# Kernel tuning notes

Hardware: AMD Instinct MI355X
Metric: run time of the kernel (lower is better)

Reference implementation:

```python
import jax, jax.numpy as jnp
import numpy as np

N = 50000
D = 128
E = 600000
R = 8


def setup_inputs() -> dict:
    key = jax.random.key(0)
    ks = jax.random.split(key, 8)
    x = jax.random.normal(ks[0], (N, D), dtype=jnp.float32)
    edge_index = jax.random.randint(ks[1], (2, E), 0, N, dtype=jnp.int64)
    edge_type = jax.random.randint(ks[2], (E,), 0, R, dtype=jnp.int64)
    scale = 1.0 / np.sqrt(D)
    w1 = jax.random.normal(ks[3], (R, D, D), dtype=jnp.float32) * scale
    root1 = jax.random.normal(ks[4], (D, D), dtype=jnp.float32) * scale
    b1 = jnp.zeros((D,), dtype=jnp.float32)
    w2 = jax.random.normal(ks[5], (R, D, D), dtype=jnp.float32) * scale
    root2 = jax.random.normal(ks[6], (D, D), dtype=jnp.float32) * scale
    b2 = jnp.zeros((D,), dtype=jnp.float32)
    return {"x": x, "edge_index": edge_index, "edge_type": edge_type,
            "w1": w1, "root1": root1, "b1": b1,
            "w2": w2, "root2": root2, "b2": b2}


def _rgcn_conv(x, edge_index, edge_type, w, root, b):
    # PyG RGCNConv: per-relation MEAN aggregation of source features over
    # incoming edges, then relation-specific linear, summed over relations,
    # plus root transform and bias.
    src, dst = edge_index[0], edge_index[1]
    # combined segment id: (dst_node, relation) -> one segment_sum pass
    seg = dst * R + edge_type  # [E]
    msgs = x[src]              # [E, D] gather
    sums = jax.ops.segment_sum(msgs, seg, num_segments=N * R).reshape(N, R, D)
    cnts = jax.ops.segment_sum(jnp.ones((msgs.shape[0],), dtype=x.dtype), seg,
                               num_segments=N * R).reshape(N, R, 1)
    mean = sums / jnp.maximum(cnts, 1.0)  # [N, R, D]; empty -> 0
    out = jnp.einsum('nrd,rde->ne', mean, w) + x @ root + b
    return out


def reference(x, edge_index, edge_type, w1, root1, b1, w2, root2, b2):
    # dropout is identity in eval mode
    h = jax.nn.relu(_rgcn_conv(x, edge_index, edge_type, w1, root1, b1))
    out = jax.nn.relu(_rgcn_conv(h, edge_index, edge_type, w2, root2, b2))
    return out
```

## Files before the change

kernel.cpp:

```cpp
#include <hip/hip_runtime.h>

#define NN 50000
#define D 128
#define EE 600000
#define R 8
#define NR (NN * R)
#define SCAN_CHUNK 1024
#define NSB ((NR + SCAN_CHUNK - 1) / SCAN_CHUNK)
#define KT 36

typedef unsigned short u16;
typedef unsigned int u32;
typedef __attribute__((ext_vector_type(8))) short bf16x8;
typedef __attribute__((ext_vector_type(4))) float f32x4;

#define RDL(v_, i_) __builtin_amdgcn_readlane((int)(v_), (i_))

__device__ inline u16 f2bf(float f) {
    union { float f; u32 u; } v; v.f = f;
    return (u16)((v.u + 0x7FFFu + ((v.u >> 16) & 1u)) >> 16);
}
__device__ inline float bf2f(u16 h) {
    union { u32 u; float f; } v; v.u = ((u32)h) << 16;
    return v.f;
}

__global__ __launch_bounds__(256) void prep2_kernel(const float4* __restrict__ x,
                                                    u32* __restrict__ xb,
                                                    const int* __restrict__ dst,
                                                    const int* __restrict__ et,
                                                    int* __restrict__ cnt,
                                                    int* __restrict__ rk) {
    const int i = blockIdx.x * 256 + threadIdx.x;
    const float4 v = x[i];
    if (i < EE) rk[i] = atomicAdd(&cnt[dst[i] * R + et[i]], 1);
    xb[i * 2] = (u32)f2bf(v.x) | ((u32)f2bf(v.y) << 16);
    xb[i * 2 + 1] = (u32)f2bf(v.z) | ((u32)f2bf(v.w) << 16);
}

__global__ __launch_bounds__(256) void scanA(const int* __restrict__ cnt,
                                             int* __restrict__ off,
                                             int* __restrict__ bsum) {
    __shared__ int ts[256];
    const int b = blockIdx.x, t = threadIdx.x;
    const int base = b * SCAN_CHUNK + t * 4;
    int v0 = 0, v1 = 0, v2 = 0, v3 = 0;
    if (base + 3 < NR) {
        int4 q = *(const int4*)(cnt + base);
        v0 = q.x; v1 = q.y; v2 = q.z; v3 = q.w;
    } else {
        if (base < NR) v0 = cnt[base];
        if (base + 1 < NR) v1 = cnt[base + 1];
        if (base + 2 < NR) v2 = cnt[base + 2];
    }
    const int s = v0 + v1 + v2 + v3;
    ts[t] = s;
    __syncthreads();
    for (int d = 1; d < 256; d <<= 1) {
        int x = (t >= d) ? ts[t - d] : 0;
        __syncthreads();
        ts[t] += x;
        __syncthreads();
    }
    const int excl = ts[t] - s;
    if (base < NR) off[base] = excl;
    if (base + 1 < NR) off[base + 1] = excl + v0;
    if (base + 2 < NR) off[base + 2] = excl + v0 + v1;
    if (base + 3 < NR) off[base + 3] = excl + v0 + v1 + v2;
    if (t == 255) bsum[b] = ts[255];
}

__global__ __launch_bounds__(256) void scanBC(int* __restrict__ off,
                                              const int* __restrict__ bsum) {
    __shared__ int red[256];
    const int b = blockIdx.x, t = threadIdx.x;
    int p = 0;
    for (int i = t; i < b; i += 256) p += bsum[i];
    red[t] = p;
    __syncthreads();
    for (int d = 128; d > 0; d >>= 1) {
        if (t < d) red[t] += red[t + d];
        __syncthreads();
    }
    const int add = red[0];
    const int base = b * SCAN_CHUNK + t * 4;
#pragma unroll
    for (int j = 0; j < 4; ++j)
        if (base + j < NR) off[base + j] += add;
    if (b == 0 && t == 0) off[NR] = EE;
}

__global__ __launch_bounds__(256) void place2_kernel(const int* __restrict__ src,
                                                     const int* __restrict__ dst,
                                                     const int* __restrict__ et,
                                                     const int* __restrict__ off,
                                                     const int* __restrict__ rk,
                                                     u32* __restrict__ epk, int E) {
    int e = blockIdx.x * 256 + threadIdx.x;
    if (e < E) {
        const int r = et[e];
        const int p = off[dst[e] * R + r] + rk[e];
        epk[p] = ((u32)src[e] << 3) | (u32)r;
    }
}

__global__ __launch_bounds__(256) void bprep2_kernel(const float* __restrict__ w1,
                                                     const float* __restrict__ root1,
                                                     u16* __restrict__ Bf1,
                                                     const float* __restrict__ w2,
                                                     const float* __restrict__ root2,
                                                     u16* __restrict__ Bf2,
                                                     int4* __restrict__ cntz) {
    int gidx = blockIdx.x * 256 + threadIdx.x;
    for (int i = gidx; i < NR / 4; i += 36864)
        cntz[i] = make_int4(0, 0, 0, 0);
    if (gidx >= 2 * KT * 8 * 64) return;
    const int layer = gidx / (KT * 8 * 64);
    const int idx = gidx - layer * (KT * 8 * 64);
    const float* w = layer ? w2 : w1;
    const float* root = layer ? root2 : root1;
    u16* Bfrag = layer ? Bf2 : Bf1;
    const int lane = idx & 63;
    const int g = (idx >> 6) & 7;
    const int kt = idx >> 9;
    const int col = g * 16 + (lane & 15);
    const int kbase = kt * 32 + (lane >> 4) * 8;
    u16* o = Bfrag + (size_t)idx * 8;
#pragma unroll
    for (int j = 0; j < 8; ++j) {
        const int k = kbase + j;
        float v = (k < R * D) ? w[(size_t)(k >> 7) * (D * D) + (size_t)(k & 127) * D + col]
                              : root[(size_t)(k - R * D) * D + col];
        o[j] = f2bf(v);
    }
}

template <bool OUTBF>
__global__ __launch_bounds__(512, 8) void rgcn_fused(const u32* __restrict__ xb,
                                                     const u16* __restrict__ Bf,
                                                     const int* __restrict__ off,
                                                     const u32* __restrict__ epk,
                                                     const float* __restrict__ bias,
                                                     void* __restrict__ outp) {
    __shared__ u32 A32[KT * 256];

    const int t = threadIdx.x;
    const int wid = t >> 6;
    const int lane = t & 63;
    const int n0 = blockIdx.x * 16;

    const int q2 = (lane & 15) >> 2;
    const int ktl = lane >> 4;
    const int xv = q2 | ((ktl & 1) << 2);

    {
        uint4* Az = (uint4*)A32;
        for (int i = t; i < (KT * 256) / 4; i += 512)
            Az[i] = make_uint4(0, 0, 0, 0);
    }
    __syncthreads();

    const int i0 = wid * 2;
    const int nb = n0 + i0;

    int offv;
    {
        int oi = nb * 8 + lane;
        if (oi > NR) oi = NR;
        offv = off[oi];
    }
    const int e0 = RDL(offv, 0);
    const int e1 = RDL(offv, 16);

    const u32 rv0 = xb[(size_t)nb * 64 + lane];
    const u32 rv1 = xb[(size_t)(nb + 1) * 64 + lane];

    int wb = e0;
    u32 w0, w1;
    {
        int ia = e0 + lane; if (ia >= EE) ia = EE - 1;
        int ib = e0 + 64 + lane; if (ib >= EE) ib = EE - 1;
        w0 = epk[ia];
        w1 = epk[ib];
    }

    int seg = 0;
    while (seg < 16 && RDL(offv, seg + 1) <= e0) ++seg;
    int segEnd = (seg < 16) ? RDL(offv, seg + 1) : 0x7FFFFFFF;
    int segStart = e0;
    float sx = 0.f, sy = 0.f;

#define FLUSH(pp)                                                              \
    do {                                                                       \
        const float inv_ = 1.f / (float)((pp) - segStart);                     \
        const int i_ = i0 + (seg >> 3);                                        \
        const int wb_ = (((i_ ^ xv) + 16 * q2) << 2) + (lane & 3);             \
        A32[((seg & 7) * 4 + ktl) * 256 + wb_] =                               \
            (u32)f2bf(sx * inv_) | ((u32)f2bf(sy * inv_) << 16);               \
        sx = 0.f; sy = 0.f; segStart = (pp);                                   \
        ++seg;                                                                 \
        while (seg < 16 && RDL(offv, seg + 1) <= (pp)) ++seg;                  \
        segEnd = (seg < 16) ? RDL(offv, seg + 1) : 0x7FFFFFFF;                 \
    } while (0)

#define PREF1(d_, pp)                                                          \
    do {                                                                       \
        const int j_ = (pp) - wb;                                              \
        const u32 pk_ = (u32)((j_ < 64) ? RDL(w0, j_) : RDL(w1, j_ - 64));     \
        d_ = xb[(size_t)(pk_ >> 3) * 64 + lane];                               \
    } while (0)

#define PROC1(v_, pp)                                                          \
    do {                                                                       \
        if ((pp) == segEnd) FLUSH(pp);                                         \
        if ((pp) < e1) {                                                       \
            union { u32 u; float f; } lo_, hi_;                                \
            lo_.u = (v_) << 16;                                                \
            hi_.u = (v_) & 0xFFFF0000u;                                        \
            sx += lo_.f;                                                       \
            sy += hi_.f;                                                       \
        }                                                                      \
    } while (0)

    int p = e0;
    u32 a0, a1, a2, a3, b0, b1, b2, b3, c0, c1, c2, c3;
    PREF1(a0, p);     PREF1(a1, p + 1); PREF1(a2, p + 2); PREF1(a3, p + 3);
    PREF1(b0, p + 4); PREF1(b1, p + 5); PREF1(b2, p + 6); PREF1(b3, p + 7);
    const int nbt = (e1 - e0 + 3) >> 2;
#pragma unroll 1
    for (int bt = 0; bt < nbt; ++bt) {
        if (p + 8 - wb >= 64) {
            wb += 64; w0 = w1;
            int ia = wb + 64 + lane; if (ia >= EE) ia = EE - 1;
            w1 = epk[ia];
        }
        PREF1(c0, p + 8); PREF1(c1, p + 9); PREF1(c2, p + 10); PREF1(c3, p + 11);
        PROC1(a0, p); PROC1(a1, p + 1); PROC1(a2, p + 2); PROC1(a3, p + 3);
        p += 4;
        a0 = b0; a1 = b1; a2 = b2; a3 = b3;
        b0 = c0; b1 = c1; b2 = c2; b3 = c3;
    }
    if (seg < 16 && segStart < e1) FLUSH(e1);

#undef FLUSH
#undef PREF1
#undef PROC1

    {
        const int wb0 = (((i0 ^ xv) + 16 * q2) << 2) + (lane & 3);
        const int wb1 = ((((i0 + 1) ^ xv) + 16 * q2) << 2) + (lane & 3);
        A32[(32 + ktl) * 256 + wb0] = rv0;
        A32[(32 + ktl) * 256 + wb1] = rv1;
    }
    __syncthreads();

    const int g = wid;
    f32x4 acc = {0.f, 0.f, 0.f, 0.f};
    const u16* bp = Bf + ((size_t)g * 64 + lane) * 8;
    const u16* A16 = (const u16*)A32;
#pragma unroll 4
    for (int kt = 0; kt < KT; ++kt) {
        const bf16x8 b = *(const bf16x8*)(bp + (size_t)kt * 4096);
        const int xvr = (lane >> 4) | ((kt & 1) << 2);
        const int lp = (lane ^ xvr) * 8;
        const bf16x8 fa = *(const bf16x8*)(A16 + kt * 512 + lp);
        acc = __builtin_amdgcn_mfma_f32_16x16x32_bf16(fa, b, acc, 0, 0, 0);
    }

    const int quad = lane >> 4;
    const int l15 = lane & 15;
    const int col = g * 16 + l15;
    const float bb = bias[col];
#pragma unroll
    for (int q = 0; q < 4; ++q) {
        const int row = n0 + quad * 4 + q;
        const float v = fmaxf(acc[q] + bb, 0.f);
        if (OUTBF)
            ((u16*)outp)[(size_t)row * D + col] = f2bf(v);
        else
            ((float*)outp)[(size_t)row * D + col] = v;
    }
}

extern "C" void kernel_launch(void* const* d_in, const int* in_sizes, int n_in,
                              void* d_out, int out_size, void* d_ws, size_t ws_size,
                              hipStream_t stream) {
    const float* x = (const float*)d_in[0];
    const int* ei = (const int*)d_in[1];
    const int* et = (const int*)d_in[2];
    const float* w1 = (const float*)d_in[3];
    const float* root1 = (const float*)d_in[4];
    const float* b1 = (const float*)d_in[5];
    const float* w2 = (const float*)d_in[6];
    const float* root2 = (const float*)d_in[7];
    const float* b2 = (const float*)d_in[8];
    float* out = (float*)d_out;

    char* ws = (char*)d_ws;
    int* off    = (int*)(ws + 0);
    int* cnt_i  = (int*)(ws + 1600512);
    int* rk     = (int*)(ws + 3200512);
    int* bsum   = (int*)(ws + 5600512);
    u32* epk    = (u32*)(ws + 5604096);
    u32* xb     = (u32*)(ws + 8004096);
    u32* h      = (u32*)(ws + 20804096);
    u16* Bf1    = (u16*)(ws + 33604096);
    u16* Bf2    = (u16*)(ws + 33899008);

    const int* srcp = ei;
    const int* dstp = ei + EE;

    bprep2_kernel<<<144, 256, 0, stream>>>(w1, root1, Bf1, w2, root2, Bf2,
                                           (int4*)cnt_i);
    prep2_kernel<<<NN * 32 / 256, 256, 0, stream>>>((const float4*)x, xb,
                                                    dstp, et, cnt_i, rk);
    scanA<<<NSB, 256, 0, stream>>>(cnt_i, off, bsum);
    scanBC<<<NSB, 256, 0, stream>>>(off, bsum);
    place2_kernel<<<(EE + 255) / 256, 256, 0, stream>>>(srcp, dstp, et, off, rk,
                                                        epk, EE);

    const int fused_blocks = NN / 16;

    rgcn_fused<true><<<fused_blocks, 512, 0, stream>>>(xb, Bf1, off, epk, b1,
                                                       (void*)h);
    rgcn_fused<false><<<fused_blocks, 512, 0, stream>>>(h, Bf2, off, epk, b2,
                                                        (void*)out);
}
```

Baseline: 252.4 us.

## Merge CSR build kernels into one cooperative kernel with grid syncs

Replaces the four preprocessing launches (convert/count, scan block, scan add, place) with a single cooperative kernel of NSB blocks that uses grid.sync between phases. It targets the launch overhead and inter-kernel gaps of the graph-preprocessing chain. In exchange, the convert and count phases now run with far fewer threads per element (grid-stride over 391 blocks), and grid-wide barriers carry their own cost. Cooperative launch also requires that all blocks be co-resident.

New measurement: 513.7 us. 104% more time.

```diff
diff --git a/kernel.cpp b/kernel.cpp
--- a/kernel.cpp
+++ b/kernel.cpp
@@ -1,4 +1,7 @@
 #include <hip/hip_runtime.h>
+#include <hip/hip_cooperative_groups.h>
+
+namespace cg = cooperative_groups;
 
 #define NN 50000
 #define D 128
@@ -23,85 +26,6 @@
 __device__ inline float bf2f(u16 h) {
     union { u32 u; float f; } v; v.u = ((u32)h) << 16;
     return v.f;
-}
-
-__global__ __launch_bounds__(256) void prep2_kernel(const float4* __restrict__ x,
-                                                    u32* __restrict__ xb,
-                                                    const int* __restrict__ dst,
-                                                    const int* __restrict__ et,
-                                                    int* __restrict__ cnt,
-                                                    int* __restrict__ rk) {
-    const int i = blockIdx.x * 256 + threadIdx.x;
-    const float4 v = x[i];
-    if (i < EE) rk[i] = atomicAdd(&cnt[dst[i] * R + et[i]], 1);
-    xb[i * 2] = (u32)f2bf(v.x) | ((u32)f2bf(v.y) << 16);
-    xb[i * 2 + 1] = (u32)f2bf(v.z) | ((u32)f2bf(v.w) << 16);
-}
-
-__global__ __launch_bounds__(256) void scanA(const int* __restrict__ cnt,
-                                             int* __restrict__ off,
-                                             int* __restrict__ bsum) {
-    __shared__ int ts[256];
-    const int b = blockIdx.x, t = threadIdx.x;
-    const int base = b * SCAN_CHUNK + t * 4;
-    int v0 = 0, v1 = 0, v2 = 0, v3 = 0;
-    if (base + 3 < NR) {
-        int4 q = *(const int4*)(cnt + base);
-        v0 = q.x; v1 = q.y; v2 = q.z; v3 = q.w;
-    } else {
-        if (base < NR) v0 = cnt[base];
-        if (base + 1 < NR) v1 = cnt[base + 1];
-        if (base + 2 < NR) v2 = cnt[base + 2];
-    }
-    const int s = v0 + v1 + v2 + v3;
-    ts[t] = s;
-    __syncthreads();
-    for (int d = 1; d < 256; d <<= 1) {
-        int x = (t >= d) ? ts[t - d] : 0;
-        __syncthreads();
-        ts[t] += x;
-        __syncthreads();
-    }
-    const int excl = ts[t] - s;
-    if (base < NR) off[base] = excl;
-    if (base + 1 < NR) off[base + 1] = excl + v0;
-    if (base + 2 < NR) off[base + 2] = excl + v0 + v1;
-    if (base + 3 < NR) off[base + 3] = excl + v0 + v1 + v2;
-    if (t == 255) bsum[b] = ts[255];
-}
-
-__global__ __launch_bounds__(256) void scanBC(int* __restrict__ off,
-                                              const int* __restrict__ bsum) {
-    __shared__ int red[256];
-    const int b = blockIdx.x, t = threadIdx.x;
-    int p = 0;
-    for (int i = t; i < b; i += 256) p += bsum[i];
-    red[t] = p;
-    __syncthreads();
-    for (int d = 128; d > 0; d >>= 1) {
-        if (t < d) red[t] += red[t + d];
-        __syncthreads();
-    }
-    const int add = red[0];
-    const int base = b * SCAN_CHUNK + t * 4;
-#pragma unroll
-    for (int j = 0; j < 4; ++j)
-        if (base + j < NR) off[base + j] += add;
-    if (b == 0 && t == 0) off[NR] = EE;
-}
-
-__global__ __launch_bounds__(256) void place2_kernel(const int* __restrict__ src,
-                                                     const int* __restrict__ dst,
-                                                     const int* __restrict__ et,
-                                                     const int* __restrict__ off,
-                                                     const int* __restrict__ rk,
-                                                     u32* __restrict__ epk, int E) {
-    int e = blockIdx.x * 256 + threadIdx.x;
-    if (e < E) {
-        const int r = et[e];
-        const int p = off[dst[e] * R + r] + rk[e];
-        epk[p] = ((u32)src[e] << 3) | (u32)r;
-    }
 }
 
 __global__ __launch_bounds__(256) void bprep2_kernel(const float* __restrict__ w1,
@@ -135,6 +59,89 @@
     }
 }
 
+__global__ __launch_bounds__(256) void prep_coop(const float4* __restrict__ x,
+                                                 u32* __restrict__ xb,
+                                                 const int* __restrict__ src,
+                                                 const int* __restrict__ dst,
+                                                 const int* __restrict__ et,
+                                                 int* __restrict__ cnt,
+                                                 int* __restrict__ rk,
+                                                 int* __restrict__ off,
+                                                 int* __restrict__ bsum,
+                                                 u32* __restrict__ epk) {
+    cg::grid_group grid = cg::this_grid();
+    __shared__ int ts[256];
+    const int b = blockIdx.x, t = threadIdx.x;
+    const int gid = b * 256 + t;
+    const int GT = NSB * 256;
+
+    for (int i = gid; i < NN * 32; i += GT) {
+        const float4 v = x[i];
+        xb[i * 2] = (u32)f2bf(v.x) | ((u32)f2bf(v.y) << 16);
+        xb[i * 2 + 1] = (u32)f2bf(v.z) | ((u32)f2bf(v.w) << 16);
+    }
+    for (int e = gid; e < EE; e += GT)
+        rk[e] = atomicAdd(&cnt[dst[e] * R + et[e]], 1);
+    __threadfence();
+    grid.sync();
+
+    {
+        const int base = b * SCAN_CHUNK + t * 4;
+        int v0 = 0, v1 = 0, v2 = 0, v3 = 0;
+        if (base + 3 < NR) {
+            int4 q = *(const int4*)(cnt + base);
+            v0 = q.x; v1 = q.y; v2 = q.z; v3 = q.w;
+        } else {
+            if (base < NR) v0 = cnt[base];
+            if (base + 1 < NR) v1 = cnt[base + 1];
+            if (base + 2 < NR) v2 = cnt[base + 2];
+        }
+        const int s = v0 + v1 + v2 + v3;
+        ts[t] = s;
+        __syncthreads();
+        for (int d = 1; d < 256; d <<= 1) {
+            int xx = (t >= d) ? ts[t - d] : 0;
+            __syncthreads();
+            ts[t] += xx;
+            __syncthreads();
+        }
+        const int excl = ts[t] - s;
+        if (base < NR) off[base] = excl;
+        if (base + 1 < NR) off[base + 1] = excl + v0;
+        if (base + 2 < NR) off[base + 2] = excl + v0 + v1;
+        if (base + 3 < NR) off[base + 3] = excl + v0 + v1 + v2;
+        if (t == 255) bsum[b] = ts[255];
+    }
+    __threadfence();
+    grid.sync();
+
+    {
+        int p = 0;
+        for (int i = t; i < b; i += 256) p += bsum[i];
+        __syncthreads();
+        ts[t] = p;
+        __syncthreads();
+        for (int d = 128; d > 0; d >>= 1) {
+            if (t < d) ts[t] += ts[t + d];
+            __syncthreads();
+        }
+        const int add = ts[0];
+        const int base = b * SCAN_CHUNK + t * 4;
+#pragma unroll
+        for (int j = 0; j < 4; ++j)
+            if (base + j < NR) off[base + j] += add;
+        if (b == 0 && t == 0) off[NR] = EE;
+    }
+    __threadfence();
+    grid.sync();
+
+    for (int e = gid; e < EE; e += GT) {
+        const int r = et[e];
+        const int p = off[dst[e] * R + r] + rk[e];
+        epk[p] = ((u32)src[e] << 3) | (u32)r;
+    }
+}
+
 template <bool OUTBF>
 __global__ __launch_bounds__(512, 8) void rgcn_fused(const u32* __restrict__ xb,
                                                      const u16* __restrict__ Bf,
@@ -312,12 +319,24 @@
 
     bprep2_kernel<<<144, 256, 0, stream>>>(w1, root1, Bf1, w2, root2, Bf2,
                                            (int4*)cnt_i);
-    prep2_kernel<<<NN * 32 / 256, 256, 0, stream>>>((const float4*)x, xb,
-                                                    dstp, et, cnt_i, rk);
-    scanA<<<NSB, 256, 0, stream>>>(cnt_i, off, bsum);
-    scanBC<<<NSB, 256, 0, stream>>>(off, bsum);
-    place2_kernel<<<(EE + 255) / 256, 256, 0, stream>>>(srcp, dstp, et, off, rk,
-                                                        epk, EE);
+
+    {
+        const float4* xf4 = (const float4*)x;
+        u32* xbp = xb;
+        const int* sp = srcp;
+        const int* dp = dstp;
+        const int* ep = et;
+        int* cp = cnt_i;
+        int* rp = rk;
+        int* op = off;
+        int* bp = bsum;
+        u32* kp = epk;
+        void* cargs[] = {(void*)&xf4, (void*)&xbp, (void*)&sp, (void*)&dp,
+                         (void*)&ep, (void*)&cp, (void*)&rp, (void*)&op,
+                         (void*)&bp, (void*)&kp};
+        hipLaunchCooperativeKernel((const void*)prep_coop, dim3(NSB), dim3(256),
+                                   cargs, 0, stream);
+    }
 
     const int fused_blocks = NN / 16;
 
```

## Use 1024-thread blocks: one node per wave, split-K MFMA across wave halves

Applied to the files above, without the earlier changes.

The fused RGCN kernel now launches 1024 threads per block so each wave gathers and averages edges for a single node instead of two. This halves the serial edge loop per wave and exposes more memory-level parallelism in the gather. The MFMA reduction over the 36 K-tiles is split across two groups of 8 waves, and the partial accumulators are combined through a new shared-memory scratch buffer after an extra barrier. In exchange it adds that barrier and scratch traffic, and the larger blocks with launch_bounds(1024,2) may limit occupancy and register budget.

Measured after the change: 276.2 us. 9.4% more time.

```diff
diff --git a/kernel.cpp b/kernel.cpp
--- a/kernel.cpp
+++ b/kernel.cpp
@@ -20,10 +20,7 @@
     union { float f; u32 u; } v; v.f = f;
     return (u16)((v.u + 0x7FFFu + ((v.u >> 16) & 1u)) >> 16);
 }
-__device__ inline float bf2f(u16 h) {
-    union { u32 u; float f; } v; v.u = ((u32)h) << 16;
-    return v.f;
-}
+
 
 __global__ __launch_bounds__(256) void prep2_kernel(const float4* __restrict__ x,
                                                     u32* __restrict__ xb,
@@ -136,13 +133,14 @@
 }
 
 template <bool OUTBF>
-__global__ __launch_bounds__(512, 8) void rgcn_fused(const u32* __restrict__ xb,
-                                                     const u16* __restrict__ Bf,
-                                                     const int* __restrict__ off,
-                                                     const u32* __restrict__ epk,
-                                                     const float* __restrict__ bias,
-                                                     void* __restrict__ outp) {
+__global__ __launch_bounds__(1024, 2) void rgcn_fused(const u32* __restrict__ xb,
+                                                      const u16* __restrict__ Bf,
+                                                      const int* __restrict__ off,
+                                                      const u32* __restrict__ epk,
+                                                      const float* __restrict__ bias,
+                                                      void* __restrict__ outp) {
     __shared__ u32 A32[KT * 256];
+    __shared__ f32x4 pscr[512];
 
     const int t = threadIdx.x;
     const int wid = t >> 6;
@@ -155,13 +153,13 @@
 
     {
         uint4* Az = (uint4*)A32;
-        for (int i = t; i < (KT * 256) / 4; i += 512)
+        for (int i = t; i < (KT * 256) / 4; i += 1024)
             Az[i] = make_uint4(0, 0, 0, 0);
     }
     __syncthreads();
 
-    const int i0 = wid * 2;
-    const int nb = n0 + i0;
+    const int iw = wid;
+    const int nb = n0 + iw;
 
     int offv;
     {
@@ -170,10 +168,9 @@
         offv = off[oi];
     }
     const int e0 = RDL(offv, 0);
-    const int e1 = RDL(offv, 16);
+    const int e1 = RDL(offv, 8);
 
     const u32 rv0 = xb[(size_t)nb * 64 + lane];
-    const u32 rv1 = xb[(size_t)(nb + 1) * 64 + lane];
 
     int wb = e0;
     u32 w0, w1;
@@ -184,23 +181,22 @@
         w1 = epk[ib];
     }
 
+    const int wbase = (((iw ^ xv) + 16 * q2) << 2) + (lane & 3);
     int seg = 0;
-    while (seg < 16 && RDL(offv, seg + 1) <= e0) ++seg;
-    int segEnd = (seg < 16) ? RDL(offv, seg + 1) : 0x7FFFFFFF;
+    while (seg < 8 && RDL(offv, seg + 1) <= e0) ++seg;
+    int segEnd = (seg < 8) ? RDL(offv, seg + 1) : 0x7FFFFFFF;
     int segStart = e0;
     float sx = 0.f, sy = 0.f;
 
 #define FLUSH(pp)                                                              \
     do {                                                                       \
         const float inv_ = 1.f / (float)((pp) - segStart);                     \
-        const int i_ = i0 + (seg >> 3);                                        \
-        const int wb_ = (((i_ ^ xv) + 16 * q2) << 2) + (lane & 3);             \
-        A32[((seg & 7) * 4 + ktl) * 256 + wb_] =                               \
+        A32[(seg * 4 + ktl) * 256 + wbase] =                                   \
             (u32)f2bf(sx * inv_) | ((u32)f2bf(sy * inv_) << 16);               \
         sx = 0.f; sy = 0.f; segStart = (pp);                                   \
         ++seg;                                                                 \
-        while (seg < 16 && RDL(offv, seg + 1) <= (pp)) ++seg;                  \
-        segEnd = (seg < 16) ? RDL(offv, seg + 1) : 0x7FFFFFFF;                 \
+        while (seg < 8 && RDL(offv, seg + 1) <= (pp)) ++seg;                   \
+        segEnd = (seg < 8) ? RDL(offv, seg + 1) : 0x7FFFFFFF;                  \
     } while (0)
 
 #define PREF1(d_, pp)                                                          \
@@ -240,45 +236,47 @@
         a0 = b0; a1 = b1; a2 = b2; a3 = b3;
         b0 = c0; b1 = c1; b2 = c2; b3 = c3;
     }
-    if (seg < 16 && segStart < e1) FLUSH(e1);
+    if (seg < 8 && segStart < e1) FLUSH(e1);
 
 #undef FLUSH
 #undef PREF1
 #undef PROC1
 
-    {
-        const int wb0 = (((i0 ^ xv) + 16 * q2) << 2) + (lane & 3);
-        const int wb1 = ((((i0 + 1) ^ xv) + 16 * q2) << 2) + (lane & 3);
-        A32[(32 + ktl) * 256 + wb0] = rv0;
-        A32[(32 + ktl) * 256 + wb1] = rv1;
-    }
-    __syncthreads();
-
-    const int g = wid;
+    A32[(32 + ktl) * 256 + wbase] = rv0;
+    __syncthreads();
+
+    const int g = wid & 7;
+    const int half = wid >> 3;
     f32x4 acc = {0.f, 0.f, 0.f, 0.f};
     const u16* bp = Bf + ((size_t)g * 64 + lane) * 8;
     const u16* A16 = (const u16*)A32;
-#pragma unroll 4
-    for (int kt = 0; kt < KT; ++kt) {
+    const int kt0 = half * 18;
+#pragma unroll
+    for (int k = 0; k < 18; ++k) {
+        const int kt = kt0 + k;
         const bf16x8 b = *(const bf16x8*)(bp + (size_t)kt * 4096);
-        const int xvr = (lane >> 4) | ((kt & 1) << 2);
+        const int xvr = (lane >> 4) | ((k & 1) << 2);
         const int lp = (lane ^ xvr) * 8;
         const bf16x8 fa = *(const bf16x8*)(A16 + kt * 512 + lp);
         acc = __builtin_amdgcn_mfma_f32_16x16x32_bf16(fa, b, acc, 0, 0, 0);
     }
-
-    const int quad = lane >> 4;
-    const int l15 = lane & 15;
-    const int col = g * 16 + l15;
-    const float bb = bias[col];
+    if (half == 1) pscr[g * 64 + lane] = acc;
+    __syncthreads();
+
+    if (half == 0) {
+        const f32x4 o = pscr[g * 64 + lane];
+        const int quad = lane >> 4;
+        const int col = g * 16 + (lane & 15);
+        const float bb = bias[col];
 #pragma unroll
-    for (int q = 0; q < 4; ++q) {
-        const int row = n0 + quad * 4 + q;
-        const float v = fmaxf(acc[q] + bb, 0.f);
-        if (OUTBF)
-            ((u16*)outp)[(size_t)row * D + col] = f2bf(v);
-        else
-            ((float*)outp)[(size_t)row * D + col] = v;
+        for (int q = 0; q < 4; ++q) {
+            const int row = n0 + quad * 4 + q;
+            const float v = fmaxf(acc[q] + o[q] + bb, 0.f);
+            if (OUTBF)
+                ((u16*)outp)[(size_t)row * D + col] = f2bf(v);
+            else
+                ((float*)outp)[(size_t)row * D + col] = v;
+        }
     }
 }
 
@@ -321,8 +319,8 @@
 
     const int fused_blocks = NN / 16;
 
-    rgcn_fused<true><<<fused_blocks, 512, 0, stream>>>(xb, Bf1, off, epk, b1,
-                                                       (void*)h);
-    rgcn_fused<false><<<fused_blocks, 512, 0, stream>>>(h, Bf2, off, epk, b2,
-                                                        (void*)out);
-}
+    rgcn_fused<true><<<fused_blocks, 1024, 0, stream>>>(xb, Bf1, off, epk, b1,
+                                                        (void*)h);
+    rgcn_fused<false><<<fused_blocks, 1024, 0, stream>>>(h, Bf2, off, epk, b2,
+                                                         (void*)out);
+}
```

## Fold preprocessing into fewer kernels, decoupled-lookback scan, fp32 gather in layer one

Applied to the files above, without the earlier changes.

The separate x-to-bf16 conversion pass is removed, so layer one gathers fp32 rows straight from x and converts only the root row. Weight fragment prep is merged into the edge-count kernel, and the two-pass scan becomes a single-pass decoupled lookback scan that also seeds per-segment cursors. Edge placement then uses atomic cursors instead of stored ranks. This saves launches and the rank and xb buffers, but layer one's gathers now move twice the bytes per edge, and edge order within a segment becomes nondeterministic.

New measurement: 287.3 us. 1.14x slower.

```diff
diff --git a/kernel.cpp b/kernel.cpp
--- a/kernel.cpp
+++ b/kernel.cpp
@@ -20,28 +20,50 @@
     union { float f; u32 u; } v; v.f = f;
     return (u16)((v.u + 0x7FFFu + ((v.u >> 16) & 1u)) >> 16);
 }
-__device__ inline float bf2f(u16 h) {
-    union { u32 u; float f; } v; v.u = ((u32)h) << 16;
-    return v.f;
-}
-
-__global__ __launch_bounds__(256) void prep2_kernel(const float4* __restrict__ x,
-                                                    u32* __restrict__ xb,
-                                                    const int* __restrict__ dst,
-                                                    const int* __restrict__ et,
-                                                    int* __restrict__ cnt,
-                                                    int* __restrict__ rk) {
-    const int i = blockIdx.x * 256 + threadIdx.x;
-    const float4 v = x[i];
-    if (i < EE) rk[i] = atomicAdd(&cnt[dst[i] * R + et[i]], 1);
-    xb[i * 2] = (u32)f2bf(v.x) | ((u32)f2bf(v.y) << 16);
-    xb[i * 2 + 1] = (u32)f2bf(v.z) | ((u32)f2bf(v.w) << 16);
-}
-
-__global__ __launch_bounds__(256) void scanA(const int* __restrict__ cnt,
+
+template <bool F32> struct LD { using T = u32; };
+template <> struct LD<true> { using T = float2; };
+
+__global__ __launch_bounds__(256) void prep_hp(const int* __restrict__ dst,
+                                               const int* __restrict__ et,
+                                               int* __restrict__ cnt,
+                                               const float* __restrict__ w1,
+                                               const float* __restrict__ root1,
+                                               u16* __restrict__ Bf1,
+                                               const float* __restrict__ w2,
+                                               const float* __restrict__ root2,
+                                               u16* __restrict__ Bf2) {
+    const int gid = blockIdx.x * 256 + threadIdx.x;
+    if (gid < EE) atomicAdd(&cnt[dst[gid] * R + et[gid]], 1);
+    if (gid < 2 * KT * 8 * 64) {
+        const int layer = gid / (KT * 8 * 64);
+        const int idx = gid - layer * (KT * 8 * 64);
+        const float* w = layer ? w2 : w1;
+        const float* root = layer ? root2 : root1;
+        u16* Bfrag = layer ? Bf2 : Bf1;
+        const int lane = idx & 63;
+        const int g = (idx >> 6) & 7;
+        const int kt = idx >> 9;
+        const int col = g * 16 + (lane & 15);
+        const int kbase = kt * 32 + (lane >> 4) * 8;
+        u16* o = Bfrag + (size_t)idx * 8;
+#pragma unroll
+        for (int j = 0; j < 8; ++j) {
+            const int k = kbase + j;
+            float v = (k < R * D)
+                          ? w[(size_t)(k >> 7) * (D * D) + (size_t)(k & 127) * D + col]
+                          : root[(size_t)(k - R * D) * D + col];
+            o[j] = f2bf(v);
+        }
+    }
+}
+
+__global__ __launch_bounds__(256) void scan1(const int* __restrict__ cnt,
                                              int* __restrict__ off,
-                                             int* __restrict__ bsum) {
+                                             int* __restrict__ cursor,
+                                             u32* __restrict__ state) {
     __shared__ int ts[256];
+    __shared__ int sbase;
     const int b = blockIdx.x, t = threadIdx.x;
     const int base = b * SCAN_CHUNK + t * 4;
     int v0 = 0, v1 = 0, v2 = 0, v3 = 0;
@@ -62,87 +84,73 @@
         ts[t] += x;
         __syncthreads();
     }
-    const int excl = ts[t] - s;
-    if (base < NR) off[base] = excl;
-    if (base + 1 < NR) off[base + 1] = excl + v0;
-    if (base + 2 < NR) off[base + 2] = excl + v0 + v1;
-    if (base + 3 < NR) off[base + 3] = excl + v0 + v1 + v2;
-    if (t == 255) bsum[b] = ts[255];
-}
-
-__global__ __launch_bounds__(256) void scanBC(int* __restrict__ off,
-                                              const int* __restrict__ bsum) {
-    __shared__ int red[256];
-    const int b = blockIdx.x, t = threadIdx.x;
-    int p = 0;
-    for (int i = t; i < b; i += 256) p += bsum[i];
-    red[t] = p;
+    const int total = ts[255];
+    if (t == 0) atomicExch(&state[b], (1u << 30) | (u32)total);
+    if (t < 64) {
+        int running = 0;
+        int wstart = b - 64;
+        for (;;) {
+            const int idx = wstart + t;
+            const u32 sv = (idx >= 0) ? atomicAdd(&state[idx], 0u) : (2u << 30);
+            const u32 fl = sv >> 30;
+            const unsigned long long binv = __ballot(fl == 0u);
+            const unsigned long long bpre = __ballot(fl == 2u);
+            if (bpre) {
+                const int hp = 63 - __builtin_clzll(bpre);
+                if (!(binv & (~0ull << hp))) {
+                    int v = (t >= hp) ? (int)(sv & 0x3FFFFFFFu) : 0;
+                    for (int o = 32; o; o >>= 1) v += __shfl_xor(v, o);
+                    running += v;
+                    break;
+                }
+            } else if (!binv) {
+                int v = (int)(sv & 0x3FFFFFFFu);
+                for (int o = 32; o; o >>= 1) v += __shfl_xor(v, o);
+                running += v;
+                wstart -= 64;
+            }
+        }
+        if (t == 0) {
+            sbase = running;
+            atomicExch(&state[b], (2u << 30) | (u32)(running + total));
+        }
+    }
     __syncthreads();
-    for (int d = 128; d > 0; d >>= 1) {
-        if (t < d) red[t] += red[t + d];
-        __syncthreads();
-    }
-    const int add = red[0];
-    const int base = b * SCAN_CHUNK + t * 4;
-#pragma unroll
-    for (int j = 0; j < 4; ++j)
-        if (base + j < NR) off[base + j] += add;
+    const int add = sbase;
+    const int excl = ts[t] - s + add;
+    if (base < NR)     { off[base] = excl;                cursor[base] = excl; }
+    if (base + 1 < NR) { off[base + 1] = excl + v0;       cursor[base + 1] = excl + v0; }
+    if (base + 2 < NR) { off[base + 2] = excl + v0 + v1;  cursor[base + 2] = excl + v0 + v1; }
+    if (base + 3 < NR) { off[base + 3] = excl + v0 + v1 + v2;
+                         cursor[base + 3] = excl + v0 + v1 + v2; }
     if (b == 0 && t == 0) off[NR] = EE;
 }
 
-__global__ __launch_bounds__(256) void place2_kernel(const int* __restrict__ src,
-                                                     const int* __restrict__ dst,
-                                                     const int* __restrict__ et,
-                                                     const int* __restrict__ off,
-                                                     const int* __restrict__ rk,
-                                                     u32* __restrict__ epk, int E) {
+__global__ __launch_bounds__(256) void place_c(const int* __restrict__ src,
+                                               const int* __restrict__ dst,
+                                               const int* __restrict__ et,
+                                               int* __restrict__ cursor,
+                                               u32* __restrict__ epk, int E) {
     int e = blockIdx.x * 256 + threadIdx.x;
     if (e < E) {
         const int r = et[e];
-        const int p = off[dst[e] * R + r] + rk[e];
+        const int p = atomicAdd(&cursor[dst[e] * R + r], 1);
         epk[p] = ((u32)src[e] << 3) | (u32)r;
     }
 }
 
-__global__ __launch_bounds__(256) void bprep2_kernel(const float* __restrict__ w1,
-                                                     const float* __restrict__ root1,
-                                                     u16* __restrict__ Bf1,
-                                                     const float* __restrict__ w2,
-                                                     const float* __restrict__ root2,
-                                                     u16* __restrict__ Bf2,
-                                                     int4* __restrict__ cntz) {
-    int gidx = blockIdx.x * 256 + threadIdx.x;
-    for (int i = gidx; i < NR / 4; i += 36864)
-        cntz[i] = make_int4(0, 0, 0, 0);
-    if (gidx >= 2 * KT * 8 * 64) return;
-    const int layer = gidx / (KT * 8 * 64);
-    const int idx = gidx - layer * (KT * 8 * 64);
-    const float* w = layer ? w2 : w1;
-    const float* root = layer ? root2 : root1;
-    u16* Bfrag = layer ? Bf2 : Bf1;
-    const int lane = idx & 63;
-    const int g = (idx >> 6) & 7;
-    const int kt = idx >> 9;
-    const int col = g * 16 + (lane & 15);
-    const int kbase = kt * 32 + (lane >> 4) * 8;
-    u16* o = Bfrag + (size_t)idx * 8;
-#pragma unroll
-    for (int j = 0; j < 8; ++j) {
-        const int k = kbase + j;
-        float v = (k < R * D) ? w[(size_t)(k >> 7) * (D * D) + (size_t)(k & 127) * D + col]
-                              : root[(size_t)(k - R * D) * D + col];
-        o[j] = f2bf(v);
-    }
-}
-
-template <bool OUTBF>
-__global__ __launch_bounds__(512, 8) void rgcn_fused(const u32* __restrict__ xb,
+template <bool INF32, bool OUTBF>
+__global__ __launch_bounds__(512, 8) void rgcn_fused(const void* __restrict__ xin,
                                                      const u16* __restrict__ Bf,
                                                      const int* __restrict__ off,
                                                      const u32* __restrict__ epk,
                                                      const float* __restrict__ bias,
                                                      void* __restrict__ outp) {
     __shared__ u32 A32[KT * 256];
+    using ldT = typename LD<INF32>::T;
+
+    const float2* xf = (const float2*)xin;
+    const u32* xu = (const u32*)xin;
 
     const int t = threadIdx.x;
     const int wid = t >> 6;
@@ -172,8 +180,16 @@
     const int e0 = RDL(offv, 0);
     const int e1 = RDL(offv, 16);
 
-    const u32 rv0 = xb[(size_t)nb * 64 + lane];
-    const u32 rv1 = xb[(size_t)(nb + 1) * 64 + lane];
+    u32 rv0, rv1;
+    if constexpr (INF32) {
+        const float2 r0 = xf[(size_t)nb * 64 + lane];
+        const float2 r1 = xf[(size_t)(nb + 1) * 64 + lane];
+        rv0 = (u32)f2bf(r0.x) | ((u32)f2bf(r0.y) << 16);
+        rv1 = (u32)f2bf(r1.x) | ((u32)f2bf(r1.y) << 16);
+    } else {
+        rv0 = xu[(size_t)nb * 64 + lane];
+        rv1 = xu[(size_t)(nb + 1) * 64 + lane];
+    }
 
     int wb = e0;
     u32 w0, w1;
@@ -207,23 +223,29 @@
     do {                                                                       \
         const int j_ = (pp) - wb;                                              \
         const u32 pk_ = (u32)((j_ < 64) ? RDL(w0, j_) : RDL(w1, j_ - 64));     \
-        d_ = xb[(size_t)(pk_ >> 3) * 64 + lane];                               \
+        if constexpr (INF32) d_ = xf[(size_t)(pk_ >> 3) * 64 + lane];          \
+        else d_ = xu[(size_t)(pk_ >> 3) * 64 + lane];                          \
     } while (0)
 
 #define PROC1(v_, pp)                                                          \
     do {                                                                       \
         if ((pp) == segEnd) FLUSH(pp);                                         \
         if ((pp) < e1) {                                                       \
-            union { u32 u; float f; } lo_, hi_;                                \
-            lo_.u = (v_) << 16;                                                \
-            hi_.u = (v_) & 0xFFFF0000u;                                        \
-            sx += lo_.f;                                                       \
-            sy += hi_.f;                                                       \
+            if constexpr (INF32) {                                             \
+                sx += (v_).x;                                                  \
+                sy += (v_).y;                                                  \
+            } else {                                                           \
+                union { u32 u; float f; } lo_, hi_;                            \
+                lo_.u = ((u32)(v_)) << 16;                                     \
+                hi_.u = ((u32)(v_)) & 0xFFFF0000u;                             \
+                sx += lo_.f;                                                   \
+                sy += hi_.f;                                                   \
+            }                                                                  \
         }                                                                      \
     } while (0)
 
     int p = e0;
-    u32 a0, a1, a2, a3, b0, b1, b2, b3, c0, c1, c2, c3;
+    ldT a0, a1, a2, a3, b0, b1, b2, b3, c0, c1, c2, c3;
     PREF1(a0, p);     PREF1(a1, p + 1); PREF1(a2, p + 2); PREF1(a3, p + 3);
     PREF1(b0, p + 4); PREF1(b1, p + 5); PREF1(b2, p + 6); PREF1(b3, p + 7);
     const int nbt = (e1 - e0 + 3) >> 2;
@@ -298,31 +320,29 @@
 
     char* ws = (char*)d_ws;
     int* off    = (int*)(ws + 0);
-    int* cnt_i  = (int*)(ws + 1600512);
-    int* rk     = (int*)(ws + 3200512);
-    int* bsum   = (int*)(ws + 5600512);
-    u32* epk    = (u32*)(ws + 5604096);
-    u32* xb     = (u32*)(ws + 8004096);
-    u32* h      = (u32*)(ws + 20804096);
-    u16* Bf1    = (u16*)(ws + 33604096);
-    u16* Bf2    = (u16*)(ws + 33899008);
+    int* cursor = (int*)(ws + 1600512);
+    int* cnt_i  = (int*)(ws + 3200512);
+    u32* state  = (u32*)(ws + 4800512);
+    u32* epk    = (u32*)(ws + 4804096);
+    u32* h      = (u32*)(ws + 7204096);
+    u16* Bf1    = (u16*)(ws + 20004096);
+    u16* Bf2    = (u16*)(ws + 20299008);
 
     const int* srcp = ei;
     const int* dstp = ei + EE;
 
-    bprep2_kernel<<<144, 256, 0, stream>>>(w1, root1, Bf1, w2, root2, Bf2,
-                                           (int4*)cnt_i);
-    prep2_kernel<<<NN * 32 / 256, 256, 0, stream>>>((const float4*)x, xb,
-                                                    dstp, et, cnt_i, rk);
-    scanA<<<NSB, 256, 0, stream>>>(cnt_i, off, bsum);
-    scanBC<<<NSB, 256, 0, stream>>>(off, bsum);
-    place2_kernel<<<(EE + 255) / 256, 256, 0, stream>>>(srcp, dstp, et, off, rk,
-                                                        epk, EE);
+    const int eblocks = (EE + 255) / 256;
+
+    hipMemsetAsync(cnt_i, 0, (size_t)NR * 4 + (size_t)NSB * 4, stream);
+    prep_hp<<<eblocks, 256, 0, stream>>>(dstp, et, cnt_i, w1, root1, Bf1,
+                                         w2, root2, Bf2);
+    scan1<<<NSB, 256, 0, stream>>>(cnt_i, off, cursor, state);
+    place_c<<<eblocks, 256, 0, stream>>>(srcp, dstp, et, cursor, epk, EE);
 
     const int fused_blocks = NN / 16;
 
-    rgcn_fused<true><<<fused_blocks, 512, 0, stream>>>(xb, Bf1, off, epk, b1,
-                                                       (void*)h);
-    rgcn_fused<false><<<fused_blocks, 512, 0, stream>>>(h, Bf2, off, epk, b2,
-                                                        (void*)out);
-}
+    rgcn_fused<true, true><<<fused_blocks, 512, 0, stream>>>(x, Bf1, off, epk,
+                                                             b1, (void*)h);
+    rgcn_fused<false, false><<<fused_blocks, 512, 0, stream>>>(h, Bf2, off, epk,
+                                                               b2, (void*)out);
+}
```
